# Performance work log

Hardware: AMD Instinct MI355X
Metric: run time of the kernel (lower is better)

The kernel has to match this reference:

```python
import jax, jax.numpy as jnp
import numpy as np

B, N, FE, FN, MD, HD, KC, P = 16, 64, 1216, 1108, 256, 256, 600, 2

def setup_inputs() -> dict:
    key = jax.random.key(0)
    ks = jax.random.split(key, 20)
    def w(k, shape, fan_in):
        return (jax.random.normal(k, shape, jnp.float32) / np.sqrt(fan_in)).astype(jnp.float32)
    return {
        "edge_features": jax.random.normal(ks[0], (B, N, N, FE), jnp.float32),
        "node_features": jax.random.normal(ks[1], (B, N, FN), jnp.float32),
        "adj_mat": jnp.zeros((B, N, N), jnp.float32),
        "node_labels": jnp.zeros((B, N, KC), jnp.float32),
        "human_nums": jnp.full((B,), 1, jnp.int32),
        "obj_nums": jnp.full((B,), N - 1, jnp.int32),
        "args": 0,
        # feature resize linears
        "W_er": w(ks[2], (MD, FE), FE), "b_er": jnp.zeros((MD,), jnp.float32),
        "W_nr": w(ks[3], (MD, FN), FN), "b_nr": jnp.zeros((MD,), jnp.float32),
        # link fun (GraphConv = stack of 1x1 conv2d): MD -> HD -> 1
        "Wl1": w(ks[4], (HD, MD), MD), "bl1": jnp.zeros((HD,), jnp.float32),
        "Wl2": w(ks[5], (1, HD), HD), "bl2": jnp.zeros((1,), jnp.float32),
        # message fun: Conv1d(2*MD -> MD, k=1) + ReLU, input = cat([h_w, e_vw])
        "Wm": w(ks[6], (MD, 2 * MD), 2 * MD), "bm": jnp.zeros((MD,), jnp.float32),
        # GRU (torch gate order r,z,n); input MD, hidden MD
        "Wi": w(ks[7], (3 * MD, MD), MD), "bi": jnp.zeros((3 * MD,), jnp.float32),
        "Wh": w(ks[8], (3 * MD, MD), MD), "bh": jnp.zeros((3 * MD,), jnp.float32),
        # readout fc
        "Wro": w(ks[9], (KC, MD), MD), "bro": jnp.zeros((KC,), jnp.float32),
    }

def reference(edge_features, node_features, adj_mat, node_labels, human_nums,
              obj_nums, args, W_er, b_er, W_nr, b_nr, Wl1, bl1, Wl2, bl2,
              Wm, bm, Wi, bi, Wh, bh, Wro, bro):
    # resize features to message size, then channel-first like torch permutes
    E0 = jnp.einsum('bvwf,mf->bmvw', edge_features, W_er) + b_er[None, :, None, None]  # [B,MD,N,N]
    Xp = jnp.einsum('bvf,mf->bmv', node_features, W_nr) + b_nr[None, :, None]           # [B,MD,N]

    # pre-mask messages are identical every round: node states are never
    # rewritten in the source and e_vw always reads the original edge_features.
    # M_pre[b,c,i,w] = relu(Wm @ cat(h_w[b,:,w], e_vw[b,:,i,w]) + bm)
    W_hw, W_ev = Wm[:, :MD], Wm[:, MD:]
    Mpre = jax.nn.relu(
        jnp.einsum('cm,bmw->bcw', W_hw, Xp)[:, :, None, :]
        + jnp.einsum('cm,bmiw->bciw', W_ev, E0)
        + bm[None, :, None, None])                                                     # [B,MD,Ni,Nw]

    E = E0  # hidden edge state, round 0
    for _ in range(P):
        h1 = jax.nn.relu(jnp.einsum('hm,bmvw->bhvw', Wl1, E) + bl1[None, :, None, None])
        A = (jnp.einsum('oh,bhvw->bovw', Wl2, h1) + bl2[None, :, None, None])[:, 0]    # [B,N,N]
        S = jax.nn.sigmoid(A)
        Mmask = Mpre * S[:, None, :, :]          # mask message i<-w by sigmoid adj[i,w]
        E = jnp.swapaxes(Mmask, 2, 3)            # E_{r+1}[b,c,w,i] = Mmask[b,c,i,w]
        m_sum = jnp.sum(Mmask, axis=3)           # [B,MD,Ni]

    # GRU update (only last round's output is read out)
    x = jnp.swapaxes(m_sum, 1, 2)                # [B,N,MD]
    h = jnp.swapaxes(Xp, 1, 2)                   # [B,N,MD]
    gi = x @ Wi.T + bi
    gh = h @ Wh.T + bh
    ir, iz, inn = jnp.split(gi, 3, axis=-1)
    hr, hz, hn = jnp.split(gh, 3, axis=-1)
    r = jax.nn.sigmoid(ir + hr)
    z = jax.nn.sigmoid(iz + hz)
    n = jnp.tanh(inn + r * hn)
    h_new = (1.0 - z) * n + z * h
    pred_node_labels = h_new @ Wro.T + bro       # [B,N,KC]
    pred_adj_mat = A                             # last round's link prediction
    return pred_adj_mat, pred_node_labels
```

## Files before the change

### kernel.cpp

```cpp
#include <hip/hip_runtime.h>
#include <cmath>

namespace {

using f16 = _Float16;
typedef f16 f16x8 __attribute__((ext_vector_type(8)));
typedef f16 f16x4 __attribute__((ext_vector_type(4)));
typedef __fp16 h16x2 __attribute__((ext_vector_type(2)));
typedef float f32x4 __attribute__((ext_vector_type(4)));

constexpr int FE = 1216, FN = 1108, MD = 256, KC = 600;
constexpr int PAIRS = 65536, ROWS = 1024;

constexpr size_t OFF_XP    = 0;
constexpr size_t OFF_XPF   = OFF_XP    + 262144;
constexpr size_t OFF_XPH   = OFF_XPF   + 131072;
constexpr size_t OFF_S1    = OFF_XPH   + 262144;
constexpr size_t OFF_S2    = OFF_S1    + 65536;
constexpr size_t OFF_XF    = OFF_S2    + 65536;
constexpr size_t OFF_GI    = OFF_XF    + 131072;
constexpr size_t OFF_GH    = OFF_GI    + 786432;
constexpr size_t OFF_HNF   = OFF_GH    + 786432;
constexpr size_t OFF_WER8  = OFF_HNF   + 131072;
constexpr size_t OFF_WNR8  = OFF_WER8  + 155648;
constexpr size_t OFF_WEV8  = OFF_WNR8  + 147456;
constexpr size_t OFF_WHW8  = OFF_WEV8  + 32768;
constexpr size_t OFF_WL18  = OFF_WHW8  + 32768;
constexpr size_t OFF_WI8   = OFF_WL18  + 32768;
constexpr size_t OFF_WH8   = OFF_WI8   + 98304;
constexpr size_t OFF_WRO8  = OFF_WH8   + 98304;
constexpr size_t OFF_E0H   = OFF_WRO8  + 98304;
constexpr size_t OFF_MPREH = OFF_E0H   + 8388608;

__device__ __forceinline__ float sigmoidf_(float x) { return 1.0f / (1.0f + expf(-x)); }

__device__ __forceinline__ void dma16(const void* g, void* l) {
  __builtin_amdgcn_global_load_lds((const unsigned int*)g, (unsigned int*)l, 16, 0, 0);
}

__device__ __forceinline__ f16x8 cvtp(f32x4 a, f32x4 b) {
  union { h16x2 q[4]; f16x8 h; } u;
  u.q[0] = __builtin_amdgcn_cvt_pkrtz(a[0], a[1]);
  u.q[1] = __builtin_amdgcn_cvt_pkrtz(a[2], a[3]);
  u.q[2] = __builtin_amdgcn_cvt_pkrtz(b[0], b[1]);
  u.q[3] = __builtin_amdgcn_cvt_pkrtz(b[2], b[3]);
  return u.h;
}

__device__ __forceinline__ f16x4 cvtp4(const float4& g) {
  union { h16x2 q[2]; f16x4 h; } u;
  u.q[0] = __builtin_amdgcn_cvt_pkrtz(g.x, g.y);
  u.q[1] = __builtin_amdgcn_cvt_pkrtz(g.z, g.w);
  return u.h;
}

__global__ __launch_bounds__(256) void cast_all(
    const float* __restrict__ W_er, const float* __restrict__ W_nr,
    const float* __restrict__ Wm,   const float* __restrict__ Wl1,
    const float* __restrict__ Wi,   const float* __restrict__ Wh,
    const float* __restrict__ Wro,
    f16* __restrict__ Wer8, f16* __restrict__ Wnr8, f16* __restrict__ Wev8,
    f16* __restrict__ Whw8, f16* __restrict__ Wl18, f16* __restrict__ Wi8,
    f16* __restrict__ Wh8,  f16* __restrict__ Wro8)
{
  int b = blockIdx.x, t = threadIdx.x;
  const float* W; f16* out; int ldw, koff, K, N, Npad, kc, nb;
  if (b < 152)      { W=W_er; out=Wer8; ldw=FE;  koff=0;   K=FE;  N=256; Npad=256; kc=b;     nb=0; }
  else if (b < 296) { b-=152; W=W_nr; out=Wnr8; ldw=FN;  koff=0;   K=FN;  N=256; Npad=256; kc=b; nb=0; }
  else if (b < 328) { b-=296; W=Wm;   out=Wev8; ldw=512; koff=256; K=256; N=256; Npad=256; kc=b; nb=0; }
  else if (b < 360) { b-=328; W=Wm;   out=Whw8; ldw=512; koff=0;   K=256; N=256; Npad=256; kc=b; nb=0; }
  else if (b < 392) { b-=360; W=Wl1;  out=Wl18; ldw=256; koff=0;   K=256; N=256; Npad=256; kc=b; nb=0; }
  else if (b < 488) { b-=392; W=Wi;   out=Wi8;  ldw=256; koff=0;   K=256; N=768; Npad=768; kc=b&31; nb=(b>>5)*256; }
  else if (b < 584) { b-=488; W=Wh;   out=Wh8;  ldw=256; koff=0;   K=256; N=768; Npad=768; kc=b&31; nb=(b>>5)*256; }
  else              { b-=584; W=Wro;  out=Wro8; ldw=256; koff=0;   K=256; N=600; Npad=768; kc=b&31; nb=(b>>5)*256; }
  int n = nb + t;
  if (n >= Npad) return;
  f16x8 h;
#pragma unroll
  for (int j = 0; j < 8; ++j) {
    int k = kc * 8 + j;
    float v = (k < K && n < N) ? W[(size_t)n * ldw + koff + k] : 0.0f;
    h[j] = (f16)v;
  }
  *reinterpret_cast<f16x8*>(out + ((size_t)kc * Npad + n) * 8) = h;
}

__global__ __launch_bounds__(256) void e0_sm(
    const float* __restrict__ A, const f16* __restrict__ Ber,
    const float* __restrict__ b_er,
    const f16* __restrict__ Bl1, const f16* __restrict__ Bev,
    const float* __restrict__ bl1, const float* __restrict__ Wl2,
    const float* __restrict__ bl2,
    const float* __restrict__ XpH, const float* __restrict__ bm,
    float* __restrict__ S1, f16* __restrict__ Mpreh)
{
  const int tid = threadIdx.x;
  const int wave = tid >> 6, l = tid & 63;
  const int lo = l & 15, hi = l >> 4;
  const int wcol = wave * 64;
  alignas(16) __shared__ char sm[49152];
  __shared__ float red[64][4];
  const size_t arow0 = (size_t)blockIdx.x * 64;

  {
    f32x4 acc[4][4] = {};
    const char* gsrc0; const char* gsrc1; const char* gsrc2; const char* gsrc3;
    int lo0, lo1, lo2, lo3;
    {
      const int colb = (l & 15) * 16;
#define E0_SRC(J, GP, LO)                                                     \
      { int row = wave*16 + (J)*4 + (l >> 4);                                 \
        int lb  = colb ^ ((row & 7) << 4);                                    \
        GP = (const char*)(A + (arow0 + row) * FE) + lb;                      \
        LO = wave*4096 + (J)*1024; }
      E0_SRC(0, gsrc0, lo0) E0_SRC(1, gsrc1, lo1)
      E0_SRC(2, gsrc2, lo2) E0_SRC(3, gsrc3, lo3)
#undef E0_SRC
    }
#define E0_ISSUE(P)                                                           \
    { char* bb = sm + (P)*16384;                                              \
      dma16(gsrc0, bb + lo0); gsrc0 += 256;                                   \
      dma16(gsrc1, bb + lo1); gsrc1 += 256;                                   \
      dma16(gsrc2, bb + lo2); gsrc2 += 256;                                   \
      dma16(gsrc3, bb + lo3); gsrc3 += 256; }

    E0_ISSUE(0)
    E0_ISSUE(1)

    for (int t = 0; t < 19; ++t) {
      if (t < 18) { asm volatile("s_waitcnt vmcnt(4)" ::: "memory"); }
      else        { asm volatile("s_waitcnt vmcnt(0)" ::: "memory"); }
      __builtin_amdgcn_sched_barrier(0);
      __builtin_amdgcn_s_barrier();
      __builtin_amdgcn_sched_barrier(0);

      f16x8 bf0[4], bf1[4];
#pragma unroll
      for (int n = 0; n < 4; ++n) {
        const int kc0 = t*8 + 0*4 + hi;
        const int kc1 = t*8 + 1*4 + hi;
        bf0[n] = *reinterpret_cast<const f16x8*>(Ber + ((size_t)kc0*256 + (wcol + n*16 + lo)) * 8);
        bf1[n] = *reinterpret_cast<const f16x8*>(Ber + ((size_t)kc1*256 + (wcol + n*16 + lo)) * 8);
      }
      __builtin_amdgcn_sched_barrier(0);
      if (t < 17) { E0_ISSUE((t + 2) % 3) }

      const char* bufp = sm + (t % 3) * 16384;
#pragma unroll
      for (int ks = 0; ks < 2; ++ks) {
        f16x8 af[4];
        const int b0 = ks*128 + hi*32;
#pragma unroll
        for (int m = 0; m < 4; ++m) {
          const int r = m*16 + lo;
          const int x = (r & 7) << 4;
          f32x4 a0 = *reinterpret_cast<const f32x4*>(bufp + r*256 + (b0 ^ x));
          f32x4 a1 = *reinterpret_cast<const f32x4*>(bufp + r*256 + ((b0 + 16) ^ x));
          af[m] = cvtp(a0, a1);
        }
#pragma unroll
        for (int m = 0; m < 4; ++m)
#pragma unroll
          for (int n = 0; n < 4; ++n)
            acc[m][n] = __builtin_amdgcn_mfma_f32_16x16x32_f16(
                af[m], ks == 0 ? bf0[n] : bf1[n], acc[m][n], 0, 0, 0);
      }
    }
#undef E0_ISSUE

    __syncthreads();
#pragma unroll
    for (int m = 0; m < 4; ++m)
#pragma unroll
      for (int n = 0; n < 4; ++n) {
        const int col = wcol + n*16 + lo;
        const float bb = b_er[col];
#pragma unroll
        for (int r = 0; r < 4; ++r) {
          const int rl = m*16 + hi*4 + r;
          const int byte = rl*512 + ((col*2) ^ ((rl & 7) << 4));
          *reinterpret_cast<f16*>(sm + byte) = (f16)(acc[m][n][r] + bb);
        }
      }
  }
  __syncthreads();

  {
    f32x4 accS[4][4] = {};
    for (int t = 0; t < 4; ++t) {
#pragma unroll
      for (int ks = 0; ks < 2; ++ks) {
        const int kc = t*8 + ks*4 + hi;
        const int b0 = t*128 + ks*64 + hi*16;
        f16x8 af[4], bf[4];
#pragma unroll
        for (int m = 0; m < 4; ++m) {
          const int r = m*16 + lo;
          af[m] = *reinterpret_cast<const f16x8*>(sm + r*512 + (b0 ^ ((r & 7) << 4)));
        }
#pragma unroll
        for (int n = 0; n < 4; ++n)
          bf[n] = *reinterpret_cast<const f16x8*>(Bl1 + ((size_t)kc*256 + (wcol + n*16 + lo)) * 8);
#pragma unroll
        for (int m = 0; m < 4; ++m)
#pragma unroll
          for (int n = 0; n < 4; ++n)
            accS[m][n] = __builtin_amdgcn_mfma_f32_16x16x32_f16(af[m], bf[n], accS[m][n], 0, 0, 0);
      }
    }
#pragma unroll
    for (int m = 0; m < 4; ++m) {
#pragma unroll
      for (int r = 0; r < 4; ++r) {
        float p = 0.f;
#pragma unroll
        for (int n = 0; n < 4; ++n) {
          const int col = wcol + n*16 + lo;
          p += Wl2[col] * fmaxf(accS[m][n][r] + bl1[col], 0.0f);
        }
        p += __shfl_xor(p, 1); p += __shfl_xor(p, 2);
        p += __shfl_xor(p, 4); p += __shfl_xor(p, 8);
        if (lo == 0) red[m*16 + hi*4 + r][wave] = p;
      }
    }
  }

  {
    f32x4 accM[4][4] = {};
    for (int t = 0; t < 4; ++t) {
#pragma unroll
      for (int ks = 0; ks < 2; ++ks) {
        const int kc = t*8 + ks*4 + hi;
        const int b0 = t*128 + ks*64 + hi*16;
        f16x8 af[4], bf[4];
#pragma unroll
        for (int m = 0; m < 4; ++m) {
          const int r = m*16 + lo;
          af[m] = *reinterpret_cast<const f16x8*>(sm + r*512 + (b0 ^ ((r & 7) << 4)));
        }
#pragma unroll
        for (int n = 0; n < 4; ++n)
          bf[n] = *reinterpret_cast<const f16x8*>(Bev + ((size_t)kc*256 + (wcol + n*16 + lo)) * 8);
#pragma unroll
        for (int m = 0; m < 4; ++m)
#pragma unroll
          for (int n = 0; n < 4; ++n)
            accM[m][n] = __builtin_amdgcn_mfma_f32_16x16x32_f16(af[m], bf[n], accM[m][n], 0, 0, 0);
      }
    }
    __syncthreads();
    const int rxb = (blockIdx.x >> 6) * 64;
#pragma unroll
    for (int m = 0; m < 4; ++m)
#pragma unroll
      for (int n = 0; n < 4; ++n) {
        const int col = wcol + n*16 + lo;
        const float bb = bm[col];
#pragma unroll
        for (int r = 0; r < 4; ++r) {
          const int rl = m*16 + hi*4 + r;
          float v = accM[m][n][r] + XpH[(size_t)(rxb + rl)*256 + col] + bb;
          *reinterpret_cast<f16*>(sm + rl*512 + col*2) = (f16)fmaxf(v, 0.0f);
        }
      }
  }
  __syncthreads();
#pragma unroll
  for (int i = 0; i < 8; ++i) {
    const int lin = i*4096 + tid*16;
    f16x8 v = *reinterpret_cast<const f16x8*>(sm + lin);
    *reinterpret_cast<f16x8*>((char*)Mpreh + arow0*512 + lin) = v;
  }
  if (tid < 64)
    S1[arow0 + tid] = sigmoidf_(bl2[0] + red[tid][0] + red[tid][1] + red[tid][2] + red[tid][3]);
}

__global__ __launch_bounds__(256) void attn2_ms(
    const f16* __restrict__ Mpreh, const float* __restrict__ S1,
    const f16* __restrict__ Bl1, const float* __restrict__ bl1,
    const float* __restrict__ Wl2, const float* __restrict__ bl2,
    float* __restrict__ adj, f16* __restrict__ xf)
{
  const int blk = blockIdx.x;
  const int b = blk >> 6, v = blk & 63;
  const int tid = threadIdx.x;
  const int wave = tid >> 6, l = tid & 63;
  const int lo = l & 15, hi = l >> 4;
  const int wcol = wave * 64;
  __shared__ f16 As[2][64][72];
  __shared__ float red[64][4];
  __shared__ float s1s[64];
  __shared__ float s2s[64];
  f32x4 acc[4][4] = {};
  const int rr0 = tid >> 3, part = tid & 7;
  const size_t pbase = (size_t)b * 4096 + v;
  f16x8 ga, gb;

  if (tid < 64) s1s[tid] = S1[pbase + (size_t)tid * 64];
  __syncthreads();

#define A2_LOAD(T)                                                              \
  { ga = *reinterpret_cast<const f16x8*>(Mpreh + (pbase + (size_t)rr0*64)*256 + (T)*64 + part*8);     \
    gb = *reinterpret_cast<const f16x8*>(Mpreh + (pbase + (size_t)(rr0+32)*64)*256 + (T)*64 + part*8); }
#define A2_WRITE(BUF)                                                           \
  { f16 sa = (f16)s1s[rr0], sb = (f16)s1s[rr0 + 32];                            \
    f16x8 ha = ga, hb = gb;                                                     \
    _Pragma("unroll") for (int j = 0; j < 8; ++j) { ha[j] *= sa; hb[j] *= sb; } \
    *reinterpret_cast<f16x8*>(&As[BUF][rr0][part*8]) = ha;                      \
    *reinterpret_cast<f16x8*>(&As[BUF][rr0 + 32][part*8]) = hb; }

  A2_LOAD(0); A2_WRITE(0);
  for (int t = 0; t < 4; ++t) {
    __syncthreads();
    if (t < 3) A2_LOAD(t + 1);
    const int cur = t & 1;
#pragma unroll
    for (int ks = 0; ks < 2; ++ks) {
      f16x8 af[4], bf[4];
      const int kc = t*8 + ks*4 + hi;
#pragma unroll
      for (int m = 0; m < 4; ++m)
        af[m] = *reinterpret_cast<const f16x8*>(&As[cur][m*16 + lo][ks*32 + hi*8]);
#pragma unroll
      for (int n = 0; n < 4; ++n)
        bf[n] = *reinterpret_cast<const f16x8*>(Bl1 + ((size_t)kc*256 + (wcol + n*16 + lo)) * 8);
#pragma unroll
      for (int m = 0; m < 4; ++m)
#pragma unroll
        for (int n = 0; n < 4; ++n)
          acc[m][n] = __builtin_amdgcn_mfma_f32_16x16x32_f16(af[m], bf[n], acc[m][n], 0, 0, 0);
    }
    if (t < 3) A2_WRITE(cur ^ 1);
  }
#undef A2_LOAD
#undef A2_WRITE
#pragma unroll
  for (int m = 0; m < 4; ++m) {
#pragma unroll
    for (int r = 0; r < 4; ++r) {
      float p = 0.f;
#pragma unroll
      for (int n = 0; n < 4; ++n) {
        const int col = wcol + n*16 + lo;
        p += Wl2[col] * fmaxf(acc[m][n][r] + bl1[col], 0.0f);
      }
      p += __shfl_xor(p, 1); p += __shfl_xor(p, 2);
      p += __shfl_xor(p, 4); p += __shfl_xor(p, 8);
      if (lo == 0) red[m*16 + hi*4 + r][wave] = p;
    }
  }
  __syncthreads();
  if (tid < 64) {
    float s = bl2[0] + red[tid][0] + red[tid][1] + red[tid][2] + red[tid][3];
    adj[(size_t)b*4096 + (size_t)v*64 + tid] = s;
    s2s[tid] = sigmoidf_(s);
  }
  __syncthreads();
  const int c = tid;
  const f16* mp = Mpreh + (size_t)blk * 64 * 256 + c;
  float accx = 0.f;
#pragma unroll 8
  for (int w = 0; w < 64; ++w)
    accx += (float)mp[(size_t)w * 256] * s2s[w];
  xf[(size_t)blk * 256 + c] = (f16)accx;
}

__global__ __launch_bounds__(256) void xp_xph16(
    const float* __restrict__ A, const f16* __restrict__ Bnr,
    const float* __restrict__ b_nr, const f16* __restrict__ Bhw,
    float* __restrict__ Xp, f16* __restrict__ Xpf, float* __restrict__ XpH)
{
  const int tid = threadIdx.x;
  const int wave = tid >> 6, l = tid & 63;
  const int lo = l & 15, hi = l >> 4;
  const int wcol = wave * 64;
  __shared__ f16 As[2][16][72];
  __shared__ f16 XpS[16][264];
  f32x4 acc[4] = {};
  const size_t arow0 = (size_t)blockIdx.x * 16;
  const int srow = tid >> 4, spart = tid & 15;
  const float* abase = A + (arow0 + srow) * FN;
  float4 g;
  const float4 z4 = make_float4(0.f, 0.f, 0.f, 0.f);

#define XQ_LOAD(T)                                                          \
  { int kb = (T)*64 + spart*4;                                              \
    g = (kb + 4 <= FN) ? *(const float4*)(abase + kb) : z4; }
#define XQ_WRITE(BUF)                                                       \
  { *reinterpret_cast<f16x4*>(&As[BUF][srow][spart*4]) = cvtp4(g); }

  XQ_LOAD(0); XQ_WRITE(0);
  for (int t = 0; t < 18; ++t) {
    __syncthreads();
    if (t < 17) XQ_LOAD(t + 1);
    const int cur = t & 1;
#pragma unroll
    for (int ks = 0; ks < 2; ++ks) {
      const int kc = t*8 + ks*4 + hi;
      f16x8 af = *reinterpret_cast<const f16x8*>(&As[cur][lo][ks*32 + hi*8]);
      f16x8 bf[4];
#pragma unroll
      for (int n = 0; n < 4; ++n)
        bf[n] = *reinterpret_cast<const f16x8*>(Bnr + ((size_t)kc*256 + (wcol + n*16 + lo)) * 8);
#pragma unroll
      for (int n = 0; n < 4; ++n)
        acc[n] = __builtin_amdgcn_mfma_f32_16x16x32_f16(af, bf[n], acc[n], 0, 0, 0);
    }
    if (t < 17) XQ_WRITE(cur ^ 1);
  }
#undef XQ_LOAD
#undef XQ_WRITE
#pragma unroll
  for (int n = 0; n < 4; ++n) {
    const int col = wcol + n*16 + lo;
    const float bb = b_nr[col];
#pragma unroll
    for (int r = 0; r < 4; ++r) {
      const size_t row = arow0 + hi*4 + r;
      float v = acc[n][r] + bb;
      Xp[row * 256 + col] = v;
      f16 hv = (f16)v;
      Xpf[row * 256 + col] = hv;
      XpS[hi*4 + r][col] = hv;
    }
  }
  __syncthreads();
  f32x4 acch[4] = {};
  for (int t = 0; t < 4; ++t) {
#pragma unroll
    for (int ks = 0; ks < 2; ++ks) {
      const int kc = t*8 + ks*4 + hi;
      f16x8 af = *reinterpret_cast<const f16x8*>(&XpS[lo][t*64 + ks*32 + hi*8]);
      f16x8 bf[4];
#pragma unroll
      for (int n = 0; n < 4; ++n)
        bf[n] = *reinterpret_cast<const f16x8*>(Bhw + ((size_t)kc*256 + (wcol + n*16 + lo)) * 8);
#pragma unroll
      for (int n = 0; n < 4; ++n)
        acch[n] = __builtin_amdgcn_mfma_f32_16x16x32_f16(af, bf[n], acch[n], 0, 0, 0);
    }
  }
#pragma unroll
  for (int n = 0; n < 4; ++n) {
    const int col = wcol + n*16 + lo;
#pragma unroll
    for (int r = 0; r < 4; ++r)
      XpH[(arow0 + hi*4 + r) * 256 + col] = acch[n][r];
  }
}

__global__ __launch_bounds__(256) void gigh16(
    const f16* __restrict__ xf, const f16* __restrict__ Xpf,
    const f16* __restrict__ Wi8, const f16* __restrict__ Wh8,
    const float* __restrict__ bi, const float* __restrict__ bh,
    float* __restrict__ gi, float* __restrict__ gh)
{
  const int rb = blockIdx.x;
  int cb = blockIdx.y;
  const f16* A; const f16* Bp; const float* bias; float* C;
  if (cb < 3) { A = xf;  Bp = Wi8; bias = bi; C = gi; }
  else        { A = Xpf; Bp = Wh8; bias = bh; C = gh; cb -= 3; }
  const int tid = threadIdx.x;
  const int wave = tid >> 6, l = tid & 63;
  const int lo = l & 15, hi = l >> 4;
  const int wcol = cb * 256 + wave * 64;
  __shared__ f16 As[16][264];
  f32x4 acc[4] = {};
  const size_t arow0 = (size_t)rb * 16;

#pragma unroll
  for (int i = 0; i < 2; ++i) {
    int idx = i * 256 + tid;
    int rr = idx >> 5, part = idx & 31;
    *reinterpret_cast<f16x8*>(&As[rr][part*8]) =
        *reinterpret_cast<const f16x8*>(A + (arow0 + rr)*256 + part*8);
  }
  __syncthreads();

  for (int t = 0; t < 4; ++t) {
#pragma unroll
    for (int ks = 0; ks < 2; ++ks) {
      const int kc = t*8 + ks*4 + hi;
      f16x8 af = *reinterpret_cast<const f16x8*>(&As[lo][t*64 + ks*32 + hi*8]);
      f16x8 bf[4];
#pragma unroll
      for (int n = 0; n < 4; ++n)
        bf[n] = *reinterpret_cast<const f16x8*>(Bp + ((size_t)kc*768 + (wcol + n*16 + lo)) * 8);
#pragma unroll
      for (int n = 0; n < 4; ++n)
        acc[n] = __builtin_amdgcn_mfma_f32_16x16x32_f16(af, bf[n], acc[n], 0, 0, 0);
    }
  }
#pragma unroll
  for (int n = 0; n < 4; ++n) {
    const int col = wcol + n*16 + lo;
    const float bb = bias[col];
#pragma unroll
    for (int r = 0; r < 4; ++r)
      C[(arow0 + hi*4 + r) * 768 + col] = acc[n][r] + bb;
  }
}

__global__ __launch_bounds__(256) void labels_gru16(
    const float* __restrict__ gi, const float* __restrict__ gh,
    const float* __restrict__ Xp, const f16* __restrict__ Wro8,
    const float* __restrict__ bro, float* __restrict__ labels)
{
  const int rb = blockIdx.x, cb = blockIdx.y;
  const int tid = threadIdx.x;
  const int wave = tid >> 6, l = tid & 63;
  const int lo = l & 15, hi = l >> 4;
  const int wcol = cb * 256 + wave * 64;
  __shared__ f16 As[16][264];
  f32x4 acc[4] = {};
  const size_t arow0 = (size_t)rb * 16;

  {
    const int rr = tid >> 4, c0 = (tid & 15) * 16;
    const float* gir = gi + (arow0 + rr) * 768;
    const float* ghr = gh + (arow0 + rr) * 768;
    const float* xpr = Xp + (arow0 + rr) * 256;
#pragma unroll
    for (int j = 0; j < 16; ++j) {
      const int c = c0 + j;
      float r = sigmoidf_(gir[c] + ghr[c]);
      float z = sigmoidf_(gir[256 + c] + ghr[256 + c]);
      float n = tanhf(gir[512 + c] + r * ghr[512 + c]);
      float h = xpr[c];
      As[rr][c] = (f16)((1.0f - z) * n + z * h);
    }
  }
  __syncthreads();

  for (int t = 0; t < 4; ++t) {
#pragma unroll
    for (int ks = 0; ks < 2; ++ks) {
      const int kc = t*8 + ks*4 + hi;
      f16x8 af = *reinterpret_cast<const f16x8*>(&As[lo][t*64 + ks*32 + hi*8]);
      f16x8 bf[4];
#pragma unroll
      for (int n = 0; n < 4; ++n)
        bf[n] = *reinterpret_cast<const f16x8*>(Wro8 + ((size_t)kc*768 + (wcol + n*16 + lo)) * 8);
#pragma unroll
      for (int n = 0; n < 4; ++n)
        acc[n] = __builtin_amdgcn_mfma_f32_16x16x32_f16(af, bf[n], acc[n], 0, 0, 0);
    }
  }
#pragma unroll
  for (int n = 0; n < 4; ++n) {
    const int col = wcol + n*16 + lo;
    if (col < KC) {
      const float bb = bro[col];
#pragma unroll
      for (int r = 0; r < 4; ++r)
        labels[(arow0 + hi*4 + r) * (size_t)KC + col] = acc[n][r] + bb;
    }
  }
}

}

extern "C" void kernel_launch(void* const* d_in, const int* in_sizes, int n_in,
                              void* d_out, int out_size, void* d_ws, size_t ws_size,
                              hipStream_t stream)
{
  const float* ef   = (const float*)d_in[0];
  const float* nf   = (const float*)d_in[1];
  const float* W_er = (const float*)d_in[7];
  const float* b_er = (const float*)d_in[8];
  const float* W_nr = (const float*)d_in[9];
  const float* b_nr = (const float*)d_in[10];
  const float* Wl1  = (const float*)d_in[11];
  const float* bl1  = (const float*)d_in[12];
  const float* Wl2  = (const float*)d_in[13];
  const float* bl2  = (const float*)d_in[14];
  const float* Wm   = (const float*)d_in[15];
  const float* bm   = (const float*)d_in[16];
  const float* Wi   = (const float*)d_in[17];
  const float* bi   = (const float*)d_in[18];
  const float* Wh   = (const float*)d_in[19];
  const float* bh   = (const float*)d_in[20];
  const float* Wro  = (const float*)d_in[21];
  const float* bro  = (const float*)d_in[22];

  float* ws = (float*)d_ws;
  float* Xp    = ws + OFF_XP;
  f16*   Xpf   = (f16*)(ws + OFF_XPF);
  float* XpH   = ws + OFF_XPH;
  float* S1    = ws + OFF_S1;
  f16*   xf    = (f16*)(ws + OFF_XF);
  float* gi    = ws + OFF_GI;
  float* gh    = ws + OFF_GH;
  f16*   Wer8  = (f16*)(ws + OFF_WER8);
  f16*   Wnr8  = (f16*)(ws + OFF_WNR8);
  f16*   Wev8  = (f16*)(ws + OFF_WEV8);
  f16*   Whw8  = (f16*)(ws + OFF_WHW8);
  f16*   Wl18  = (f16*)(ws + OFF_WL18);
  f16*   Wi8   = (f16*)(ws + OFF_WI8);
  f16*   Wh8   = (f16*)(ws + OFF_WH8);
  f16*   Wro8  = (f16*)(ws + OFF_WRO8);
  f16*   Mpreh = (f16*)(ws + OFF_MPREH);
  float* adj    = (float*)d_out;
  float* labels = (float*)d_out + PAIRS;

  dim3 blk(256);

  cast_all<<<dim3(680), blk, 0, stream>>>(W_er, W_nr, Wm, Wl1, Wi, Wh, Wro,
                                          Wer8, Wnr8, Wev8, Whw8, Wl18, Wi8, Wh8, Wro8);
  xp_xph16<<<dim3(64), blk, 0, stream>>>(nf, Wnr8, b_nr, Whw8, Xp, Xpf, XpH);
  e0_sm<<<dim3(PAIRS / 64), blk, 0, stream>>>(ef, Wer8, b_er, Wl18, Wev8,
                                              bl1, Wl2, bl2, XpH, bm,
                                              S1, Mpreh);
  attn2_ms<<<dim3(PAIRS / 64), blk, 0, stream>>>(Mpreh, S1, Wl18, bl1, Wl2, bl2,
                                                 adj, xf);
  gigh16<<<dim3(64, 6), blk, 0, stream>>>(xf, Xpf, Wi8, Wh8, bi, bh, gi, gh);
  labels_gru16<<<dim3(64, 3), blk, 0, stream>>>(gi, gh, Xp, Wro8, bro, labels);
}
```

Baseline: 203.3 us.

## Replace LDS triple-buffered DMA pipeline with direct global loads in edge GEMM

The edge-feature GEMM stage no longer stages A tiles into LDS through async global_load_lds with a triple buffer and barriers. Each wave now loads its A fragments straight from global memory into registers and converts them to fp16 before the MFMAs. This cuts LDS use from 48KB to 32KB and drops the per-iteration barriers. In exchange, the four waves load the same A rows redundantly from global/L2, and the explicit prefetch that overlapped loads with compute is lost.

Result: slower. 316.8 us (+55.9%).

```diff
diff --git a/kernel.cpp b/kernel.cpp
--- a/kernel.cpp
+++ b/kernel.cpp
@@ -34,10 +34,6 @@
 
 __device__ __forceinline__ float sigmoidf_(float x) { return 1.0f / (1.0f + expf(-x)); }
 
-__device__ __forceinline__ void dma16(const void* g, void* l) {
-  __builtin_amdgcn_global_load_lds((const unsigned int*)g, (unsigned int*)l, 16, 0, 0);
-}
-
 __device__ __forceinline__ f16x8 cvtp(f32x4 a, f32x4 b) {
   union { h16x2 q[4]; f16x8 h; } u;
   u.q[0] = __builtin_amdgcn_cvt_pkrtz(a[0], a[1]);
@@ -98,77 +94,40 @@
   const int wave = tid >> 6, l = tid & 63;
   const int lo = l & 15, hi = l >> 4;
   const int wcol = wave * 64;
-  alignas(16) __shared__ char sm[49152];
+  alignas(16) __shared__ char sm[32768];
   __shared__ float red[64][4];
   const size_t arow0 = (size_t)blockIdx.x * 64;
 
   {
     f32x4 acc[4][4] = {};
-    const char* gsrc0; const char* gsrc1; const char* gsrc2; const char* gsrc3;
-    int lo0, lo1, lo2, lo3;
-    {
-      const int colb = (l & 15) * 16;
-#define E0_SRC(J, GP, LO)                                                     \
-      { int row = wave*16 + (J)*4 + (l >> 4);                                 \
-        int lb  = colb ^ ((row & 7) << 4);                                    \
-        GP = (const char*)(A + (arow0 + row) * FE) + lb;                      \
-        LO = wave*4096 + (J)*1024; }
-      E0_SRC(0, gsrc0, lo0) E0_SRC(1, gsrc1, lo1)
-      E0_SRC(2, gsrc2, lo2) E0_SRC(3, gsrc3, lo3)
-#undef E0_SRC
-    }
-#define E0_ISSUE(P)                                                           \
-    { char* bb = sm + (P)*16384;                                              \
-      dma16(gsrc0, bb + lo0); gsrc0 += 256;                                   \
-      dma16(gsrc1, bb + lo1); gsrc1 += 256;                                   \
-      dma16(gsrc2, bb + lo2); gsrc2 += 256;                                   \
-      dma16(gsrc3, bb + lo3); gsrc3 += 256; }
-
-    E0_ISSUE(0)
-    E0_ISSUE(1)
+    const char* abase[4];
+#pragma unroll
+    for (int m = 0; m < 4; ++m)
+      abase[m] = (const char*)(A + (arow0 + m*16 + lo) * FE) + hi*32;
 
     for (int t = 0; t < 19; ++t) {
-      if (t < 18) { asm volatile("s_waitcnt vmcnt(4)" ::: "memory"); }
-      else        { asm volatile("s_waitcnt vmcnt(0)" ::: "memory"); }
-      __builtin_amdgcn_sched_barrier(0);
-      __builtin_amdgcn_s_barrier();
-      __builtin_amdgcn_sched_barrier(0);
-
-      f16x8 bf0[4], bf1[4];
-#pragma unroll
-      for (int n = 0; n < 4; ++n) {
-        const int kc0 = t*8 + 0*4 + hi;
-        const int kc1 = t*8 + 1*4 + hi;
-        bf0[n] = *reinterpret_cast<const f16x8*>(Ber + ((size_t)kc0*256 + (wcol + n*16 + lo)) * 8);
-        bf1[n] = *reinterpret_cast<const f16x8*>(Ber + ((size_t)kc1*256 + (wcol + n*16 + lo)) * 8);
-      }
-      __builtin_amdgcn_sched_barrier(0);
-      if (t < 17) { E0_ISSUE((t + 2) % 3) }
-
-      const char* bufp = sm + (t % 3) * 16384;
 #pragma unroll
       for (int ks = 0; ks < 2; ++ks) {
-        f16x8 af[4];
-        const int b0 = ks*128 + hi*32;
+        const int kc = t*8 + ks*4 + hi;
+        f16x8 af[4], bf[4];
 #pragma unroll
         for (int m = 0; m < 4; ++m) {
-          const int r = m*16 + lo;
-          const int x = (r & 7) << 4;
-          f32x4 a0 = *reinterpret_cast<const f32x4*>(bufp + r*256 + (b0 ^ x));
-          f32x4 a1 = *reinterpret_cast<const f32x4*>(bufp + r*256 + ((b0 + 16) ^ x));
+          const char* p = abase[m] + t*256 + ks*128;
+          f32x4 a0 = *reinterpret_cast<const f32x4*>(p);
+          f32x4 a1 = *reinterpret_cast<const f32x4*>(p + 16);
           af[m] = cvtp(a0, a1);
         }
 #pragma unroll
+        for (int n = 0; n < 4; ++n)
+          bf[n] = *reinterpret_cast<const f16x8*>(Ber + ((size_t)kc*256 + (wcol + n*16 + lo)) * 8);
+#pragma unroll
         for (int m = 0; m < 4; ++m)
 #pragma unroll
           for (int n = 0; n < 4; ++n)
-            acc[m][n] = __builtin_amdgcn_mfma_f32_16x16x32_f16(
-                af[m], ks == 0 ? bf0[n] : bf1[n], acc[m][n], 0, 0, 0);
-      }
-    }
-#undef E0_ISSUE
-
-    __syncthreads();
+            acc[m][n] = __builtin_amdgcn_mfma_f32_16x16x32_f16(af[m], bf[n], acc[m][n], 0, 0, 0);
+      }
+    }
+
 #pragma unroll
     for (int m = 0; m < 4; ++m)
 #pragma unroll
```
